# Kernel optimization log

Hardware: AMD Instinct MI355X
Metric: run time of the kernel (lower is better)

Reference implementation:

```python
import jax, jax.numpy as jnp
import numpy as np

B, C, H, W = 1, 12, 256, 256
T = 8          # time_steps
F = 64         # recurrent/conv filters
SIGMA = 1.0


def _to_c(x):
    return jax.lax.complex(x[..., 0], x[..., 1])


def _to_r(x):
    return jnp.stack([jnp.real(x), jnp.imag(x)], axis=-1)


def _fft2c(x):  # orthogonal centered 2D FFT over last two dims (complex input)
    x = jnp.fft.ifftshift(x, axes=(-2, -1))
    x = jnp.fft.fft2(x, axes=(-2, -1), norm='ortho')
    return jnp.fft.fftshift(x, axes=(-2, -1))


def _ifft2c(x):
    x = jnp.fft.ifftshift(x, axes=(-2, -1))
    x = jnp.fft.ifft2(x, axes=(-2, -1), norm='ortho')
    return jnp.fft.fftshift(x, axes=(-2, -1))


def _conv(x, w, b=None, dilation=1):
    k = w.shape[-1]
    pad = dilation * (k - 1) // 2  # 'same' padding as ConvNonlinear
    y = jax.lax.conv_general_dilated(x, w, (1, 1), [(pad, pad), (pad, pad)],
                                     rhs_dilation=(dilation, dilation),
                                     dimension_numbers=('NCHW', 'OIHW', 'NCHW'))
    if b is not None:
        y = y + b[None, :, None, None]
    return y


def _gru(x, h, ih_w, ih_b, hh_w, hh_b):  # ConvGRUCell
    i_r, i_z, i_n = jnp.split(_conv(x, ih_w, ih_b), 3, axis=1)
    h_r, h_z, h_n = jnp.split(_conv(h, hh_w, hh_b), 3, axis=1)
    r = jax.nn.sigmoid(i_r + h_r)
    z = jax.nn.sigmoid(i_z + h_z)
    n = jnp.tanh(i_n + r * h_n)
    return (1.0 - z) * n + z * h


def setup_inputs():
    key = jax.random.key(0)
    ks = jax.random.split(key, 16)
    rn = lambda k, s, sc=1.0: jax.random.normal(k, s, jnp.float32) * sc
    return {
        'pred': rn(ks[0], (B, C, H, W, 2)),
        'masked_kspace': rn(ks[1], (B, C, H, W, 2)),
        'sense': rn(ks[2], (B, C, H, W, 2), 0.1),
        'mask': jax.random.randint(ks[3], (B, 1, H, W, 1), 0, 2).astype(bool),
        'conv1_w': rn(ks[4], (F, 4, 5, 5), 0.05),
        'conv1_b': jnp.zeros((F,), jnp.float32),
        'gru1_ih_w': rn(ks[5], (3 * F, F, 1, 1), 0.05),
        'gru1_ih_b': jnp.zeros((3 * F,), jnp.float32),
        'gru1_hh_w': rn(ks[6], (3 * F, F, 1, 1), 0.05),
        'gru1_hh_b': jnp.zeros((3 * F,), jnp.float32),
        'conv2_w': rn(ks[7], (F, F, 3, 3), 0.05),
        'conv2_b': jnp.zeros((F,), jnp.float32),
        'gru2_ih_w': rn(ks[8], (3 * F, F, 1, 1), 0.05),
        'gru2_ih_b': jnp.zeros((3 * F,), jnp.float32),
        'gru2_hh_w': rn(ks[9], (3 * F, F, 1, 1), 0.05),
        'gru2_hh_b': jnp.zeros((3 * F,), jnp.float32),
        'final_w': rn(ks[10], (2, F, 3, 3), 0.05),
        'dc_weight': jnp.ones((1,), jnp.float32),
    }


def reference(pred, masked_kspace, sense, mask, conv1_w, conv1_b, gru1_ih_w, gru1_ih_b,
              gru1_hh_w, gru1_hh_b, conv2_w, conv2_b, gru2_ih_w, gru2_ih_b, gru2_hh_w,
              gru2_hh_b, final_w, dc_weight):
    ksp_c = _to_c(masked_kspace)   # [B,C,H,W] complex
    sense_c = _to_c(sense)
    mask_f = mask[..., 0].astype(jnp.float32)  # [B,1,H,W]
    # eta init (eta=None path): coil-combined ifft of pred
    eta0 = jnp.sum(_ifft2c(_to_c(pred)) * jnp.conj(sense_c), axis=1)  # [B,H,W]
    h1_0 = jnp.zeros((B, F, H, W), jnp.float32)
    h2_0 = jnp.zeros((B, F, H, W), jnp.float32)
    inv_s2 = 1.0 / (SIGMA * SIGMA)

    def step(carry, _):
        eta, h1, h2 = carry
        # log_likelihood_gradient: SENSE-expand, fft, masked residual, ifft, coil-combine
        resid = _ifft2c(mask_f * (_fft2c(eta[:, None] * sense_c) - ksp_c))  # [B,C,H,W]
        grad = jnp.sum(resid * jnp.conj(sense_c), axis=1)                   # [B,H,W]
        g = jnp.stack([eta.real, eta.imag, grad.real, grad.imag], axis=1) * inv_s2  # [B,4,H,W]
        h1 = _gru(jax.nn.relu(_conv(g, conv1_w, conv1_b, 1)), h1,
                  gru1_ih_w, gru1_ih_b, gru1_hh_w, gru1_hh_b)
        h2 = _gru(jax.nn.relu(_conv(h1, conv2_w, conv2_b, 2)), h2,
                  gru2_ih_w, gru2_ih_b, gru2_hh_w, gru2_hh_b)
        d = _conv(h2, final_w, None, 1)  # [B,2,H,W], no bias, no nonlinearity
        eta = eta + jax.lax.complex(d[:, 0], d[:, 1])
        return (eta, h1, h2), eta

    _, etas = jax.lax.scan(step, (eta0, h1_0, h2_0), None, length=T)  # [T,B,H,W]
    # data-consistency output per time step
    soft_dc = jnp.where(mask, pred - masked_kspace, 0.0) * dc_weight[0]  # [B,C,H,W,2]
    dc_c = _to_c(soft_dc)
    out = ksp_c[None] - dc_c[None] - _fft2c(etas[:, :, None] * sense_c[None])  # [T,B,C,H,W]
    return _to_r(out)  # [T,B,C,H,W,2]
```

## Files before the change

### kernel.cpp

```cpp
#include <hip/hip_runtime.h>

#define HW 65536
#define NC 12
#define NF 64
#define NT 8
#define P2 260

typedef float2 c32;
typedef __attribute__((ext_vector_type(8))) short bf16x8;
typedef __attribute__((ext_vector_type(4))) float f32x4;

__device__ __forceinline__ float ssign(int p) {
    return ((p ^ (p >> 8)) & 1) ? -1.0f : 1.0f;
}

__device__ __forceinline__ short f2bf(float f) {
    union { float f; unsigned u; } v; v.f = f;
    unsigned r = (v.u + 0x7FFFu + ((v.u >> 16) & 1u)) >> 16;
    return (short)r;
}

__device__ __forceinline__ float bf2f(unsigned short u) {
    union { unsigned u; float f; } v; v.u = (unsigned)u << 16;
    return v.f;
}

__device__ __forceinline__ void wave_sync() {
    asm volatile("s_waitcnt lgkmcnt(0)" ::: "memory");
}

__device__ __forceinline__ void fft256_wave(c32* X, const c32* tw, int j, float conjf) {
    #pragma unroll
    for (int s = 1; s <= 8; s += 2) {
        const int H = 1 << (s - 1);
        int p = j & (H - 1);
        int r = j >> (s - 1);
        int i0 = r * 4 * H + p;
        c32 e0 = X[i0], e1 = X[i0 + H], e2 = X[i0 + 2 * H], e3 = X[i0 + 3 * H];
        c32 w = tw[p << (8 - s)];
        float wy = conjf * w.y;
        c32 t = make_float2(w.x * e1.x - wy * e1.y, w.x * e1.y + wy * e1.x);
        c32 a0 = make_float2(e0.x + t.x, e0.y + t.y);
        c32 a1 = make_float2(e0.x - t.x, e0.y - t.y);
        t = make_float2(w.x * e3.x - wy * e3.y, w.x * e3.y + wy * e3.x);
        c32 a2 = make_float2(e2.x + t.x, e2.y + t.y);
        c32 a3 = make_float2(e2.x - t.x, e2.y - t.y);
        c32 w0 = tw[p << (7 - s)];
        c32 w1 = tw[(p + H) << (7 - s)];
        float w0y = conjf * w0.y, w1y = conjf * w1.y;
        t = make_float2(w0.x * a2.x - w0y * a2.y, w0.x * a2.y + w0y * a2.x);
        X[i0]         = make_float2(a0.x + t.x, a0.y + t.y);
        X[i0 + 2 * H] = make_float2(a0.x - t.x, a0.y - t.y);
        t = make_float2(w1.x * a3.x - w1y * a3.y, w1.x * a3.y + w1y * a3.x);
        X[i0 + H]     = make_float2(a1.x + t.x, a1.y + t.y);
        X[i0 + 3 * H] = make_float2(a1.x - t.x, a1.y - t.y);
        wave_sync();
    }
}

__device__ __forceinline__ void fft256_2w(c32* X, const c32* tw, int lane, float conjf) {
    #pragma unroll
    for (int s = 1; s <= 8; ++s) {
        const int half = 1 << (s - 1);
        int grp = lane >> (s - 1);
        int pos = lane & (half - 1);
        int i0 = (grp << s) + pos;
        int i1 = i0 + half;
        c32 w = tw[pos << (8 - s)];
        float wy = conjf * w.y;
        c32 a = X[i0], cc = X[i1];
        c32 t = make_float2(w.x * cc.x - wy * cc.y, w.x * cc.y + wy * cc.x);
        X[i0] = make_float2(a.x + t.x, a.y + t.y);
        X[i1] = make_float2(a.x - t.x, a.y - t.y);
        __syncthreads();
    }
}

__device__ __forceinline__ void build_tw(c32* tw, int tid) {
    if (tid < 128) {
        float a = -3.14159265358979323846f * (float)tid * (1.0f / 128.0f);
        float sv, cv;
        sincosf(a, &sv, &cv);
        tw[tid] = make_float2(cv, sv);
    }
}

__global__ __launch_bounds__(256) void fft_rows_pre(c32* __restrict__ buf,
        const c32* __restrict__ pred) {
    __shared__ c32 lds[2][256];
    __shared__ c32 tw[128];
    int tid = threadIdx.x;
    build_tw(tw, tid);
    int li = tid >> 7, lane = tid & 127;
    int r = blockIdx.x * 2 + li;
    int coil = r >> 8, y = r & 255;
    c32* rp = buf + (size_t)r * 256;
    c32* X = lds[li];
    #pragma unroll
    for (int e = 0; e < 2; ++e) {
        int n = (e << 7) + lane;
        float s = ((n + y) & 1) ? -1.0f : 1.0f;
        c32 pv = pred[(size_t)coil * HW + y * 256 + n];
        X[__brev((unsigned)n) >> 24] = make_float2(s * pv.x, s * pv.y);
    }
    __syncthreads();
    fft256_2w(X, tw, lane, -1.0f);
    #pragma unroll
    for (int e = 0; e < 2; ++e) {
        int n = (e << 7) + lane;
        rp[n] = X[n];
    }
}

__global__ __launch_bounds__(256) void fft_rows_exp(c32* __restrict__ buf,
        const c32* __restrict__ eta, const c32* __restrict__ sense) {
    __shared__ c32 lds[2][256];
    __shared__ c32 tw[128];
    int tid = threadIdx.x;
    build_tw(tw, tid);
    int li = tid >> 7, lane = tid & 127;
    int r = blockIdx.x * 2 + li;
    int coil = r >> 8, y = r & 255;
    c32* rp = buf + (size_t)r * 256;
    c32* X = lds[li];
    #pragma unroll
    for (int e = 0; e < 2; ++e) {
        int n = (e << 7) + lane;
        float s = ((n + y) & 1) ? -1.0f : 1.0f;
        c32 ev = eta[y * 256 + n];
        c32 sn = sense[(size_t)coil * HW + y * 256 + n];
        X[__brev((unsigned)n) >> 24] =
            make_float2(s * (ev.x * sn.x - ev.y * sn.y),
                        s * (ev.x * sn.y + ev.y * sn.x));
    }
    __syncthreads();
    fft256_2w(X, tw, lane, 1.0f);
    #pragma unroll
    for (int e = 0; e < 2; ++e) {
        int n = (e << 7) + lane;
        rp[n] = X[n];
    }
}

__global__ __launch_bounds__(768) void final_exp(const short* __restrict__ hTp,
        const short* __restrict__ wA, c32* __restrict__ eta,
        const c32* __restrict__ sense, c32* __restrict__ buf) {
    __shared__ c32 X[12][256];
    __shared__ c32 tw[128];
    __shared__ float erx[256], ery[256];
    int tid = threadIdx.x;
    build_tw(tw, tid);
    int wv = tid >> 6, l = tid & 63;
    int lr = l & 15, lg = l >> 4;
    int y = blockIdx.x;

    for (int tile = wv; tile < 16; tile += 12) {
        int x = tile * 16 + lr;
        f32x4 C = (f32x4){0.f, 0.f, 0.f, 0.f};
        #pragma unroll
        for (int tap = 0; tap < 9; ++tap) {
            int dy = tap / 3 - 1, dx = tap % 3 - 1;
            const short* pA = wA + (size_t)(tap * 16 + lr) * 64 + lg * 8;
            bf16x8 A0 = *(const bf16x8*)(pA);
            bf16x8 A1 = *(const bf16x8*)(pA + 32);
            const short* pB = hTp +
                ((size_t)((y + dy + 2) * P2 + (x + dx + 2)) << 6) + lg * 8;
            bf16x8 B0 = *(const bf16x8*)(pB);
            bf16x8 B1 = *(const bf16x8*)(pB + 32);
            C = __builtin_amdgcn_mfma_f32_16x16x32_bf16(A0, B0, C, 0, 0, 0);
            C = __builtin_amdgcn_mfma_f32_16x16x32_bf16(A1, B1, C, 0, 0, 0);
        }
        if (lg == 0) {
            int px = y * 256 + x;
            c32 e = eta[px];
            float ex = e.x + C[0], ey = e.y + C[1];
            eta[px] = make_float2(ex, ey);
            erx[x] = ex; ery[x] = ey;
        }
    }
    __syncthreads();

    {
        c32* Xc = &X[wv][0];
        const c32* sn = sense + (size_t)wv * HW + y * 256;
        #pragma unroll
        for (int e = 0; e < 4; ++e) {
            int n = (e << 6) + l;
            float s = ((n + y) & 1) ? -1.0f : 1.0f;
            float ex = erx[n], ey = ery[n];
            c32 sv = sn[n];
            Xc[__brev((unsigned)n) >> 24] =
                make_float2(s * (ex * sv.x - ey * sv.y),
                            s * (ex * sv.y + ey * sv.x));
        }
        wave_sync();
        fft256_wave(Xc, tw, l, 1.0f);
        c32* rp = buf + (size_t)wv * HW + y * 256;
        #pragma unroll
        for (int e = 0; e < 4; ++e) {
            int n = (e << 6) + l;
            rp[n] = Xc[n];
        }
    }
}

__global__ __launch_bounds__(768) void fft_rows_grad(const c32* __restrict__ Fk,
        const c32* __restrict__ sense, const c32* __restrict__ eta,
        short* __restrict__ gTp) {
    __shared__ c32 lds[12][256];
    __shared__ c32 tw[128];
    int tid = threadIdx.x;
    build_tw(tw, tid);
    int wid = tid >> 6, j = tid & 63;
    int y = blockIdx.x;
    {
        const c32* rp = Fk + (size_t)wid * HW + y * 256;
        #pragma unroll
        for (int e = 0; e < 4; ++e) {
            int n = (e << 6) + j;
            lds[wid][__brev((unsigned)n) >> 24] = rp[n];
        }
    }
    __syncthreads();
    fft256_wave(&lds[wid][0], tw, j, -1.0f);
    __syncthreads();
    if (tid < 256) {
        int x = tid;
        int p = y * 256 + x;
        float ax = 0.f, ay = 0.f;
        #pragma unroll
        for (int c = 0; c < NC; ++c) {
            c32 t = lds[c][x];
            c32 s = sense[(size_t)c * HW + p];
            ax += t.x * s.x + t.y * s.y;
            ay += t.y * s.x - t.x * s.y;
        }
        float sc = (((x + y) & 1) ? -1.0f : 1.0f) * (1.0f / 256.0f);
        c32 e = eta[p];
        ushort4 o;
        o.x = (unsigned short)f2bf(e.x);
        o.y = (unsigned short)f2bf(e.y);
        o.z = (unsigned short)f2bf(ax * sc);
        o.w = (unsigned short)f2bf(ay * sc);
        ((ushort4*)gTp)[(y + 2) * P2 + x + 2] = o;
    }
}

__global__ __launch_bounds__(1024) void fft_cols(c32* __restrict__ buf, float conjf) {
    __shared__ c32 lds[8][257];
    __shared__ c32 tw[128];
    int tid = threadIdx.x;
    build_tw(tw, tid);
    c32* ip = buf + (size_t)blockIdx.y * HW;
    int x0 = blockIdx.x * 8;
    int xl = tid & 7, yb = tid >> 3;
    #pragma unroll
    for (int e = 0; e < 2; ++e) {
        int y = yb + (e << 7);
        lds[xl][__brev((unsigned)y) >> 24] = ip[y * 256 + x0 + xl];
    }
    __syncthreads();
    int col = tid >> 7, lane = tid & 127;
    fft256_2w(&lds[col][0], tw, lane, conjf);
    #pragma unroll
    for (int e = 0; e < 2; ++e) {
        int y = yb + (e << 7);
        ip[y * 256 + x0 + xl] = lds[xl][y];
    }
}

__global__ __launch_bounds__(1024) void fft_cols_fused(c32* __restrict__ buf,
        const c32* __restrict__ base, const c32* __restrict__ ksp,
        const int* __restrict__ mask, c32* __restrict__ outp, int write_out) {
    __shared__ c32 lds[8][257];
    __shared__ c32 tw[128];
    int tid = threadIdx.x;
    build_tw(tw, tid);
    int coil = blockIdx.y;
    c32* ip = buf + (size_t)coil * HW;
    int x0 = blockIdx.x * 8;
    int xl = tid & 7, yb = tid >> 3;
    #pragma unroll
    for (int e = 0; e < 2; ++e) {
        int y = yb + (e << 7);
        lds[xl][__brev((unsigned)y) >> 24] = ip[y * 256 + x0 + xl];
    }
    __syncthreads();
    int col = tid >> 7, lane = tid & 127;
    fft256_2w(&lds[col][0], tw, lane, 1.0f);

    int x = x0 + xl;
    c32 G[2];
    #pragma unroll
    for (int e = 0; e < 2; ++e) {
        int y = yb + (e << 7);
        G[e] = lds[xl][y];
    }
    __syncthreads();
    #pragma unroll
    for (int e = 0; e < 2; ++e) {
        int y = yb + (e << 7);
        int p = y * 256 + x;
        size_t i = (size_t)coil * HW + p;
        float s = ((p ^ (p >> 8)) & 1) ? -1.0f : 1.0f;
        if (write_out) {
            c32 bv = base[i];
            float sc = s * (1.0f / 256.0f);
            outp[i] = make_float2(bv.x - sc * G[e].x, bv.y - sc * G[e].y);
        }
        c32 rv = make_float2(0.f, 0.f);
        if (mask[p]) {
            c32 k = ksp[i];
            rv = make_float2(G[e].x * (1.0f / 256.0f) - s * k.x,
                             G[e].y * (1.0f / 256.0f) - s * k.y);
        }
        lds[xl][__brev((unsigned)y) >> 24] = rv;
    }
    __syncthreads();
    fft256_2w(&lds[col][0], tw, lane, -1.0f);
    #pragma unroll
    for (int e = 0; e < 2; ++e) {
        int y = yb + (e << 7);
        ip[y * 256 + x0 + xl] = lds[xl][y];
    }
}

__global__ __launch_bounds__(256) void k_combine_eta0(const c32* __restrict__ tmp,
        const c32* __restrict__ sense, c32* __restrict__ eta) {
    int p = blockIdx.x * 256 + threadIdx.x;
    float ax = 0.f, ay = 0.f;
    for (int c = 0; c < NC; ++c) {
        c32 t = tmp[c * HW + p], s = sense[c * HW + p];
        ax += t.x * s.x + t.y * s.y;
        ay += t.y * s.x - t.x * s.y;
    }
    float sc = ssign(p) * (1.0f / 256.0f);
    eta[p] = make_float2(ax * sc, ay * sc);
}

__global__ __launch_bounds__(256) void k_base(const c32* __restrict__ ksp,
        const c32* __restrict__ pred, const int* __restrict__ mask,
        const float* __restrict__ dcw, c32* __restrict__ base) {
    int i = blockIdx.x * 256 + threadIdx.x;
    int p = i & (HW - 1);
    c32 k = ksp[i];
    c32 o = k;
    if (mask[p]) {
        float w = dcw[0];
        c32 pr = pred[i];
        o.x -= (pr.x - k.x) * w;
        o.y -= (pr.y - k.y) * w;
    }
    base[i] = o;
}

__global__ __launch_bounds__(256) void k_zero_border(short* __restrict__ gTp,
        short* __restrict__ h1a, short* __restrict__ h1b,
        short* __restrict__ h2a, short* __restrict__ h2b) {
    int i = blockIdx.x * 256 + threadIdx.x;
    if (i >= 2064) return;
    int y, x;
    if (i < 1040) {
        int r = i / 260;
        y = (r < 2) ? r : 256 + r;
        x = i % 260;
    } else {
        int j = i - 1040;
        y = 2 + (j >> 2);
        int cix = j & 3;
        x = (cix < 2) ? cix : 256 + cix;
    }
    size_t px = (size_t)y * P2 + x;
    ((ushort4*)gTp)[px] = make_ushort4(0, 0, 0, 0);
    uint4 z = make_uint4(0, 0, 0, 0);
    uint4* p1 = (uint4*)(h1a + (px << 6));
    uint4* p2 = (uint4*)(h1b + (px << 6));
    uint4* p3 = (uint4*)(h2a + (px << 6));
    uint4* p4 = (uint4*)(h2b + (px << 6));
    #pragma unroll
    for (int e = 0; e < 8; ++e) { p1[e] = z; p2[e] = z; p3[e] = z; p4[e] = z; }
}

__global__ __launch_bounds__(256) void k_prep_c1(const float* __restrict__ w,
        short* __restrict__ wA) {
    int i = blockIdx.x * 256 + threadIdx.x;
    int co = i >> 7, k = i & 127;
    int tap = k >> 2, ci = k & 3;
    float v = (tap < 25) ? w[co * 100 + ci * 25 + tap] : 0.f;
    wA[i] = f2bf(v);
}

__global__ __launch_bounds__(256) void k_prep_c2(const float* __restrict__ w,
        short* __restrict__ wA) {
    int i = blockIdx.x * 256 + threadIdx.x;
    int tap = i >> 12, co = (i >> 6) & 63, ci = i & 63;
    wA[i] = f2bf(w[co * 576 + ci * 9 + tap]);
}

__global__ __launch_bounds__(256) void k_prep_cf(const float* __restrict__ w,
        short* __restrict__ wA) {
    int i = blockIdx.x * 256 + threadIdx.x;
    int tap = i >> 10, r = (i >> 6) & 15, ci = i & 63;
    float v = (r < 2) ? w[r * 576 + ci * 9 + tap] : 0.f;
    wA[i] = f2bf(v);
}

__global__ __launch_bounds__(128) void k_prep_gru(const float* __restrict__ ihw,
        const float* __restrict__ ihb, const float* __restrict__ hhw,
        const float* __restrict__ hhb, short* __restrict__ w2, float* __restrict__ bias) {
    int k = threadIdx.x;
    int r = blockIdx.x;
    int g = r >> 6, co = r & 63;
    float v = 0.f;
    if (g == 0)      v = (k < 64) ? ihw[co * 64 + k]         : hhw[co * 64 + k - 64];
    else if (g == 1) v = (k < 64) ? ihw[(64 + co) * 64 + k]  : hhw[(64 + co) * 64 + k - 64];
    else if (g == 2) v = (k < 64) ? ihw[(128 + co) * 64 + k] : 0.f;
    else             v = (k < 64) ? 0.f : hhw[(128 + co) * 64 + k - 64];
    w2[r * 128 + k] = f2bf(v);
    if (k == 0) {
        float b = (g == 0) ? ihb[co] + hhb[co]
                : (g == 1) ? ihb[64 + co] + hhb[64 + co]
                : (g == 2) ? ihb[128 + co] : hhb[128 + co];
        bias[r] = b;
    }
}

template <int NTN, bool FIRST>
__device__ __forceinline__ void gru_tail(const short (*xch)[68],
        const short* __restrict__ hprev, const short* __restrict__ w2,
        const float* __restrict__ bias, short* __restrict__ hnext,
        int wv, int lr, int lg, int px0) {
    bf16x8 A0[4], A1[4], A2[2], A3[2];
    {
        const short* w0 = w2 + (0   + wv * 16 + lr) * 128 + lg * 8;
        const short* w1 = w2 + (64  + wv * 16 + lr) * 128 + lg * 8;
        const short* w2p = w2 + (128 + wv * 16 + lr) * 128 + lg * 8;
        const short* w3 = w2 + (192 + wv * 16 + lr) * 128 + lg * 8;
        #pragma unroll
        for (int kt = 0; kt < 4; ++kt) {
            A0[kt] = *(const bf16x8*)(w0 + kt * 32);
            A1[kt] = *(const bf16x8*)(w1 + kt * 32);
        }
        A2[0] = *(const bf16x8*)(w2p);          A2[1] = *(const bf16x8*)(w2p + 32);
        A3[0] = *(const bf16x8*)(w3 + 64);      A3[1] = *(const bf16x8*)(w3 + 96);
    }

    f32x4 C0[NTN], C1[NTN], C2[NTN], C3[NTN];
    #pragma unroll
    for (int nt = 0; nt < NTN; ++nt) {
        C0[nt] = (f32x4){0.f, 0.f, 0.f, 0.f};
        C1[nt] = (f32x4){0.f, 0.f, 0.f, 0.f};
        C2[nt] = (f32x4){0.f, 0.f, 0.f, 0.f};
        C3[nt] = (f32x4){0.f, 0.f, 0.f, 0.f};
    }

    #pragma unroll
    for (int nt = 0; nt < NTN; ++nt) {
        int pxl = nt * 16 + lr;
        int px = px0 + pxl;
        int yy = px >> 8, xx = px & 255;
        size_t pb = ((size_t)((yy + 2) * P2 + (xx + 2)) << 6);
        bf16x8 B0 = *(const bf16x8*)&xch[pxl][lg * 8];
        bf16x8 B1 = *(const bf16x8*)&xch[pxl][32 + lg * 8];
        C0[nt] = __builtin_amdgcn_mfma_f32_16x16x32_bf16(A0[0], B0, C0[nt], 0, 0, 0);
        C0[nt] = __builtin_amdgcn_mfma_f32_16x16x32_bf16(A0[1], B1, C0[nt], 0, 0, 0);
        C1[nt] = __builtin_amdgcn_mfma_f32_16x16x32_bf16(A1[0], B0, C1[nt], 0, 0, 0);
        C1[nt] = __builtin_amdgcn_mfma_f32_16x16x32_bf16(A1[1], B1, C1[nt], 0, 0, 0);
        C2[nt] = __builtin_amdgcn_mfma_f32_16x16x32_bf16(A2[0], B0, C2[nt], 0, 0, 0);
        C2[nt] = __builtin_amdgcn_mfma_f32_16x16x32_bf16(A2[1], B1, C2[nt], 0, 0, 0);
        if (!FIRST) {
            bf16x8 B2 = *(const bf16x8*)(hprev + pb + lg * 8);
            bf16x8 B3 = *(const bf16x8*)(hprev + pb + 32 + lg * 8);
            C0[nt] = __builtin_amdgcn_mfma_f32_16x16x32_bf16(A0[2], B2, C0[nt], 0, 0, 0);
            C0[nt] = __builtin_amdgcn_mfma_f32_16x16x32_bf16(A0[3], B3, C0[nt], 0, 0, 0);
            C1[nt] = __builtin_amdgcn_mfma_f32_16x16x32_bf16(A1[2], B2, C1[nt], 0, 0, 0);
            C1[nt] = __builtin_amdgcn_mfma_f32_16x16x32_bf16(A1[3], B3, C1[nt], 0, 0, 0);
            C3[nt] = __builtin_amdgcn_mfma_f32_16x16x32_bf16(A3[0], B2, C3[nt], 0, 0, 0);
            C3[nt] = __builtin_amdgcn_mfma_f32_16x16x32_bf16(A3[1], B3, C3[nt], 0, 0, 0);
        }
    }

    int co = wv * 16 + lg * 4;
    float br[4], bz[4], bin_[4], bhn[4];
    #pragma unroll
    for (int i = 0; i < 4; ++i) {
        br[i]   = bias[co + i];
        bz[i]   = bias[64 + co + i];
        bin_[i] = bias[128 + co + i];
        bhn[i]  = bias[192 + co + i];
    }
    #pragma unroll
    for (int nt = 0; nt < NTN; ++nt) {
        int px = px0 + nt * 16 + lr;
        int yy = px >> 8, xx = px & 255;
        size_t pb = ((size_t)((yy + 2) * P2 + (xx + 2)) << 6);
        ushort4 hov = make_ushort4(0, 0, 0, 0);
        if (!FIRST) hov = *(const ushort4*)(hprev + pb + co);
        float ho[4] = {bf2f(hov.x), bf2f(hov.y), bf2f(hov.z), bf2f(hov.w)};
        ushort4 st;
        unsigned short* sp = &st.x;
        #pragma unroll
        for (int i = 0; i < 4; ++i) {
            float r = 1.0f / (1.0f + expf(-(C0[nt][i] + br[i])));
            float z = 1.0f / (1.0f + expf(-(C1[nt][i] + bz[i])));
            float nn = tanhf(C2[nt][i] + bin_[i] + r * (C3[nt][i] + bhn[i]));
            float hv = FIRST ? (1.0f - z) * nn : (1.0f - z) * nn + z * ho[i];
            sp[i] = (unsigned short)f2bf(hv);
        }
        *(ushort4*)(hnext + pb + co) = st;
    }
}

template <bool FIRST>
__global__ __launch_bounds__(256, 2) void conv1_gru1(const short* __restrict__ gTp,
        const short* __restrict__ wA, const float* __restrict__ cbias,
        const short* __restrict__ w2, const float* __restrict__ gbias,
        const short* __restrict__ hprev, short* __restrict__ hnext) {
    __shared__ short xch[32][68];
    int wv = threadIdx.x >> 6, l = threadIdx.x & 63;
    int lr = l & 15, lg = l >> 4;
    int y = blockIdx.x >> 3;
    int x0 = (blockIdx.x & 7) << 5;

    bf16x8 A[4];
    const short* pA = wA + (size_t)(wv * 16 + lr) * 128 + lg * 8;
    #pragma unroll
    for (int kt = 0; kt < 4; ++kt) A[kt] = *(const bf16x8*)(pA + kt * 32);

    bf16x8 B[2][4];
    #pragma unroll
    for (int nt = 0; nt < 2; ++nt) {
        int x = x0 + nt * 16 + lr;
        #pragma unroll
        for (int kt = 0; kt < 4; ++kt) {
            int t0 = kt * 8 + lg * 2;
            #pragma unroll
            for (int half = 0; half < 2; ++half) {
                int tap = t0 + half;
                int tt = (tap < 25) ? tap : 0;
                int dy = tt / 5 - 2, dx = tt % 5 - 2;
                ushort4 v = *(const ushort4*)(gTp +
                    ((size_t)((y + dy + 2) * P2 + (x + dx + 2)) << 2));
                B[nt][kt][half * 4 + 0] = (short)v.x;
                B[nt][kt][half * 4 + 1] = (short)v.y;
                B[nt][kt][half * 4 + 2] = (short)v.z;
                B[nt][kt][half * 4 + 3] = (short)v.w;
            }
        }
    }
    int co = wv * 16 + lg * 4;
    #pragma unroll
    for (int nt = 0; nt < 2; ++nt) {
        f32x4 C = (f32x4){0.f, 0.f, 0.f, 0.f};
        #pragma unroll
        for (int kt = 0; kt < 4; ++kt)
            C = __builtin_amdgcn_mfma_f32_16x16x32_bf16(A[kt], B[nt][kt], C, 0, 0, 0);
        ushort4 st;
        st.x = (unsigned short)f2bf(fmaxf(C[0] + cbias[co + 0], 0.f));
        st.y = (unsigned short)f2bf(fmaxf(C[1] + cbias[co + 1], 0.f));
        st.z = (unsigned short)f2bf(fmaxf(C[2] + cbias[co + 2], 0.f));
        st.w = (unsigned short)f2bf(fmaxf(C[3] + cbias[co + 3], 0.f));
        *(ushort4*)&xch[nt * 16 + lr][co] = st;
    }
    __syncthreads();

    gru_tail<2, FIRST>(xch, hprev, w2, gbias, hnext, wv, lr, lg, y * 256 + x0);
}

template <bool FIRST>
__global__ __launch_bounds__(256, 2) void conv2_gru2(const short* __restrict__ h1Tp,
        const short* __restrict__ wA, const float* __restrict__ cbias,
        const short* __restrict__ w2, const float* __restrict__ gbias,
        const short* __restrict__ hprev, short* __restrict__ hnext) {
    __shared__ uint4 Ld[3][68][9];
    __shared__ short xch[64][68];
    int tid = threadIdx.x;
    int wv = tid >> 6, l = tid & 63;
    int lr = l & 15, lg = l >> 4;
    int y = blockIdx.x >> 2;
    int x0 = (blockIdx.x & 3) << 6;

    for (int n = tid; n < 3 * 68 * 8; n += 256) {
        int r = n / (68 * 8);
        int rem = n - r * (68 * 8);
        int px = rem >> 3, e = rem & 7;
        const uint4* src = (const uint4*)(h1Tp +
            (((size_t)(y + 2 * r) * P2 + (x0 + px)) << 6)) + e;
        Ld[r][px][e] = *src;
    }
    __syncthreads();

    f32x4 C[4];
    #pragma unroll
    for (int nt = 0; nt < 4; ++nt) C[nt] = (f32x4){0.f, 0.f, 0.f, 0.f};

    #pragma unroll
    for (int tap = 0; tap < 9; ++tap) {
        int r = tap / 3;
        int dx = (tap % 3 - 1) * 2;
        const short* pA = wA + (size_t)(tap * 64 + wv * 16 + lr) * 64 + lg * 8;
        bf16x8 A0 = *(const bf16x8*)(pA);
        bf16x8 A1 = *(const bf16x8*)(pA + 32);
        #pragma unroll
        for (int nt = 0; nt < 4; ++nt) {
            int xl = nt * 16 + lr + dx + 2;
            bf16x8 B0 = *(const bf16x8*)&Ld[r][xl][lg];
            bf16x8 B1 = *(const bf16x8*)&Ld[r][xl][4 + lg];
            C[nt] = __builtin_amdgcn_mfma_f32_16x16x32_bf16(A0, B0, C[nt], 0, 0, 0);
            C[nt] = __builtin_amdgcn_mfma_f32_16x16x32_bf16(A1, B1, C[nt], 0, 0, 0);
        }
    }
    int co = wv * 16 + lg * 4;
    #pragma unroll
    for (int nt = 0; nt < 4; ++nt) {
        ushort4 st;
        st.x = (unsigned short)f2bf(fmaxf(C[nt][0] + cbias[co + 0], 0.f));
        st.y = (unsigned short)f2bf(fmaxf(C[nt][1] + cbias[co + 1], 0.f));
        st.z = (unsigned short)f2bf(fmaxf(C[nt][2] + cbias[co + 2], 0.f));
        st.w = (unsigned short)f2bf(fmaxf(C[nt][3] + cbias[co + 3], 0.f));
        *(ushort4*)&xch[nt * 16 + lr][co] = st;
    }
    __syncthreads();

    gru_tail<4, FIRST>(xch, hprev, w2, gbias, hnext, wv, lr, lg, y * 256 + x0);
}

extern "C" void kernel_launch(void* const* d_in, const int* in_sizes, int n_in,
                              void* d_out, int out_size, void* d_ws, size_t ws_size,
                              hipStream_t stream) {
    const c32* pred   = (const c32*)d_in[0];
    const c32* ksp    = (const c32*)d_in[1];
    const c32* sense  = (const c32*)d_in[2];
    const int* mask   = (const int*)d_in[3];
    const float* c1w  = (const float*)d_in[4];
    const float* c1b  = (const float*)d_in[5];
    const float* g1iw = (const float*)d_in[6];
    const float* g1ib = (const float*)d_in[7];
    const float* g1hw = (const float*)d_in[8];
    const float* g1hb = (const float*)d_in[9];
    const float* c2w  = (const float*)d_in[10];
    const float* c2b  = (const float*)d_in[11];
    const float* g2iw = (const float*)d_in[12];
    const float* g2ib = (const float*)d_in[13];
    const float* g2hw = (const float*)d_in[14];
    const float* g2hb = (const float*)d_in[15];
    const float* fw   = (const float*)d_in[16];
    const float* dcw  = (const float*)d_in[17];

    const size_t PP = (size_t)P2 * P2;
    float* w0 = (float*)d_ws;
    c32* base = (c32*)w0;
    c32* Fk   = base + NC * HW;
    c32* tmp  = Fk + NC * HW;
    c32* eta  = tmp + NC * HW;
    short* gTp = (short*)(eta + HW);
    short* h1Ta = gTp + PP * 4;
    short* h1Tb = h1Ta + PP * 64;
    short* h2Ta = h1Tb + PP * 64;
    short* h2Tb = h2Ta + PP * 64;
    short* w2a  = h2Tb + PP * 64;
    short* w2b  = w2a + 256 * 128;
    float* biasA = (float*)(w2b + 256 * 128);
    float* biasB = biasA + 256;
    short* wAc2 = (short*)(biasB + 256);
    short* wAc1 = wAc2 + 9 * 64 * 64;
    short* wAcf = wAc1 + 64 * 128;

    dim3 B(256);
    const int gCHW = NC * HW / 256;
    const int gHW  = HW / 256;
    const int gROW = NC * 256 / 2;
    dim3 gCOL(32, NC);
    dim3 B1024(1024);
    dim3 B768(768);
    const int gC1 = HW / 32;
    const int gC2 = HW / 64;

    k_zero_border<<<9, B, 0, stream>>>(gTp, h1Ta, h1Tb, h2Ta, h2Tb);
    k_prep_gru<<<256, 128, 0, stream>>>(g1iw, g1ib, g1hw, g1hb, w2a, biasA);
    k_prep_gru<<<256, 128, 0, stream>>>(g2iw, g2ib, g2hw, g2hb, w2b, biasB);
    k_prep_c2<<<144, 256, 0, stream>>>(c2w, wAc2);
    k_prep_c1<<<32, 256, 0, stream>>>(c1w, wAc1);
    k_prep_cf<<<36, 256, 0, stream>>>(fw, wAcf);

    fft_rows_pre<<<gROW, B, 0, stream>>>(tmp, pred);
    fft_cols<<<gCOL, B1024, 0, stream>>>(tmp, -1.0f);
    k_combine_eta0<<<gHW, B, 0, stream>>>(tmp, sense, eta);

    k_base<<<gCHW, B, 0, stream>>>(ksp, pred, mask, dcw, base);

    fft_rows_exp<<<gROW, B, 0, stream>>>(Fk, eta, sense);
    fft_cols_fused<<<gCOL, B1024, 0, stream>>>(Fk, base, ksp, mask, (c32*)d_out, 0);

    short* h1c = h1Ta; short* h1n = h1Tb;
    short* h2c = h2Ta; short* h2n = h2Tb;
    c32* outp = (c32*)d_out;

    for (int t = 0; t < NT; ++t) {
        fft_rows_grad<<<gHW, B768, 0, stream>>>(Fk, sense, eta, gTp);

        if (t == 0) {
            conv1_gru1<true><<<gC1, B, 0, stream>>>(gTp, wAc1, c1b, w2a, biasA, h1c, h1n);
        } else {
            conv1_gru1<false><<<gC1, B, 0, stream>>>(gTp, wAc1, c1b, w2a, biasA, h1c, h1n);
        }
        { short* s = h1c; h1c = h1n; h1n = s; }
        if (t == 0) {
            conv2_gru2<true><<<gC2, B, 0, stream>>>(h1c, wAc2, c2b, w2b, biasB, h2c, h2n);
        } else {
            conv2_gru2<false><<<gC2, B, 0, stream>>>(h1c, wAc2, c2b, w2b, biasB, h2c, h2n);
        }
        { short* s = h2c; h2c = h2n; h2n = s; }

        final_exp<<<gHW, B768, 0, stream>>>(h2c, wAcf, eta, sense, Fk);

        fft_cols_fused<<<gCOL, B1024, 0, stream>>>(Fk, base, ksp, mask,
                                                   outp + (size_t)t * NC * HW, 1);
    }
}
```

Measured before the change: 853.0 us.

## Store k-space intermediate and sense maps as packed bf16 complex

Stores the per-coil k-space intermediate buffer (Fk) and a precomputed copy of the sense maps as packed bf16 pairs, one 32-bit word per complex value, in place of float2. All row/column FFT kernels in the loop now read and write half the bytes. The aim is to cut global memory traffic in these bandwidth-bound FFT passes. The cost is lower precision in the FFT intermediates and coil combination, which can affect accuracy of the outputs written at each step.

```diff
diff --git a/kernel.cpp b/kernel.cpp
--- a/kernel.cpp
+++ b/kernel.cpp
@@ -23,6 +23,16 @@
 __device__ __forceinline__ float bf2f(unsigned short u) {
     union { unsigned u; float f; } v; v.u = (unsigned)u << 16;
     return v.f;
+}
+
+__device__ __forceinline__ unsigned pack_bf(float x, float y) {
+    return (unsigned)(unsigned short)f2bf(x) |
+           ((unsigned)(unsigned short)f2bf(y) << 16);
+}
+
+__device__ __forceinline__ c32 unpack_bf(unsigned u) {
+    return make_float2(bf2f((unsigned short)(u & 0xffff)),
+                       bf2f((unsigned short)(u >> 16)));
 }
 
 __device__ __forceinline__ void wave_sync() {
@@ -112,7 +122,7 @@
     }
 }
 
-__global__ __launch_bounds__(256) void fft_rows_exp(c32* __restrict__ buf,
+__global__ __launch_bounds__(256) void fft_rows_exp(unsigned* __restrict__ buf,
         const c32* __restrict__ eta, const c32* __restrict__ sense) {
     __shared__ c32 lds[2][256];
     __shared__ c32 tw[128];
@@ -121,7 +131,7 @@
     int li = tid >> 7, lane = tid & 127;
     int r = blockIdx.x * 2 + li;
     int coil = r >> 8, y = r & 255;
-    c32* rp = buf + (size_t)r * 256;
+    unsigned* rp = buf + (size_t)r * 256;
     c32* X = lds[li];
     #pragma unroll
     for (int e = 0; e < 2; ++e) {
@@ -138,13 +148,13 @@
     #pragma unroll
     for (int e = 0; e < 2; ++e) {
         int n = (e << 7) + lane;
-        rp[n] = X[n];
+        rp[n] = pack_bf(X[n].x, X[n].y);
     }
 }
 
 __global__ __launch_bounds__(768) void final_exp(const short* __restrict__ hTp,
         const short* __restrict__ wA, c32* __restrict__ eta,
-        const c32* __restrict__ sense, c32* __restrict__ buf) {
+        const unsigned* __restrict__ senseb, unsigned* __restrict__ buf) {
     __shared__ c32 X[12][256];
     __shared__ c32 tw[128];
     __shared__ float erx[256], ery[256];
@@ -182,30 +192,30 @@
 
     {
         c32* Xc = &X[wv][0];
-        const c32* sn = sense + (size_t)wv * HW + y * 256;
+        const unsigned* sn = senseb + (size_t)wv * HW + y * 256;
         #pragma unroll
         for (int e = 0; e < 4; ++e) {
             int n = (e << 6) + l;
             float s = ((n + y) & 1) ? -1.0f : 1.0f;
             float ex = erx[n], ey = ery[n];
-            c32 sv = sn[n];
+            c32 sv = unpack_bf(sn[n]);
             Xc[__brev((unsigned)n) >> 24] =
                 make_float2(s * (ex * sv.x - ey * sv.y),
                             s * (ex * sv.y + ey * sv.x));
         }
         wave_sync();
         fft256_wave(Xc, tw, l, 1.0f);
-        c32* rp = buf + (size_t)wv * HW + y * 256;
+        unsigned* rp = buf + (size_t)wv * HW + y * 256;
         #pragma unroll
         for (int e = 0; e < 4; ++e) {
             int n = (e << 6) + l;
-            rp[n] = Xc[n];
-        }
-    }
-}
-
-__global__ __launch_bounds__(768) void fft_rows_grad(const c32* __restrict__ Fk,
-        const c32* __restrict__ sense, const c32* __restrict__ eta,
+            rp[n] = pack_bf(Xc[n].x, Xc[n].y);
+        }
+    }
+}
+
+__global__ __launch_bounds__(768) void fft_rows_grad(const unsigned* __restrict__ Fk,
+        const unsigned* __restrict__ senseb, const c32* __restrict__ eta,
         short* __restrict__ gTp) {
     __shared__ c32 lds[12][256];
     __shared__ c32 tw[128];
@@ -214,11 +224,11 @@
     int wid = tid >> 6, j = tid & 63;
     int y = blockIdx.x;
     {
-        const c32* rp = Fk + (size_t)wid * HW + y * 256;
+        const unsigned* rp = Fk + (size_t)wid * HW + y * 256;
         #pragma unroll
         for (int e = 0; e < 4; ++e) {
             int n = (e << 6) + j;
-            lds[wid][__brev((unsigned)n) >> 24] = rp[n];
+            lds[wid][__brev((unsigned)n) >> 24] = unpack_bf(rp[n]);
         }
     }
     __syncthreads();
@@ -231,7 +241,7 @@
         #pragma unroll
         for (int c = 0; c < NC; ++c) {
             c32 t = lds[c][x];
-            c32 s = sense[(size_t)c * HW + p];
+            c32 s = unpack_bf(senseb[(size_t)c * HW + p]);
             ax += t.x * s.x + t.y * s.y;
             ay += t.y * s.x - t.x * s.y;
         }
@@ -269,7 +279,7 @@
     }
 }
 
-__global__ __launch_bounds__(1024) void fft_cols_fused(c32* __restrict__ buf,
+__global__ __launch_bounds__(1024) void fft_cols_fused(unsigned* __restrict__ buf,
         const c32* __restrict__ base, const c32* __restrict__ ksp,
         const int* __restrict__ mask, c32* __restrict__ outp, int write_out) {
     __shared__ c32 lds[8][257];
@@ -277,13 +287,13 @@
     int tid = threadIdx.x;
     build_tw(tw, tid);
     int coil = blockIdx.y;
-    c32* ip = buf + (size_t)coil * HW;
+    unsigned* ip = buf + (size_t)coil * HW;
     int x0 = blockIdx.x * 8;
     int xl = tid & 7, yb = tid >> 3;
     #pragma unroll
     for (int e = 0; e < 2; ++e) {
         int y = yb + (e << 7);
-        lds[xl][__brev((unsigned)y) >> 24] = ip[y * 256 + x0 + xl];
+        lds[xl][__brev((unsigned)y) >> 24] = unpack_bf(ip[y * 256 + x0 + xl]);
     }
     __syncthreads();
     int col = tid >> 7, lane = tid & 127;
@@ -321,7 +331,7 @@
     #pragma unroll
     for (int e = 0; e < 2; ++e) {
         int y = yb + (e << 7);
-        ip[y * 256 + x0 + xl] = lds[xl][y];
+        ip[y * 256 + x0 + xl] = pack_bf(lds[xl][y].x, lds[xl][y].y);
     }
 }
 
@@ -352,6 +362,13 @@
         o.y -= (pr.y - k.y) * w;
     }
     base[i] = o;
+}
+
+__global__ __launch_bounds__(256) void k_prep_sense(const c32* __restrict__ sense,
+        unsigned* __restrict__ senseb) {
+    int i = blockIdx.x * 256 + threadIdx.x;
+    c32 s = sense[i];
+    senseb[i] = pack_bf(s.x, s.y);
 }
 
 __global__ __launch_bounds__(256) void k_zero_border(short* __restrict__ gTp,
@@ -650,10 +667,11 @@
     const size_t PP = (size_t)P2 * P2;
     float* w0 = (float*)d_ws;
     c32* base = (c32*)w0;
-    c32* Fk   = base + NC * HW;
-    c32* tmp  = Fk + NC * HW;
+    c32* tmp  = base + NC * HW;
     c32* eta  = tmp + NC * HW;
-    short* gTp = (short*)(eta + HW);
+    unsigned* Fkb = (unsigned*)(eta + HW);
+    unsigned* senseb = Fkb + NC * HW;
+    short* gTp = (short*)(senseb + NC * HW);
     short* h1Ta = gTp + PP * 4;
     short* h1Tb = h1Ta + PP * 64;
     short* h2Ta = h1Tb + PP * 64;
@@ -682,6 +700,7 @@
     k_prep_c2<<<144, 256, 0, stream>>>(c2w, wAc2);
     k_prep_c1<<<32, 256, 0, stream>>>(c1w, wAc1);
     k_prep_cf<<<36, 256, 0, stream>>>(fw, wAcf);
+    k_prep_sense<<<gCHW, B, 0, stream>>>(sense, senseb);
 
     fft_rows_pre<<<gROW, B, 0, stream>>>(tmp, pred);
     fft_cols<<<gCOL, B1024, 0, stream>>>(tmp, -1.0f);
@@ -689,15 +708,15 @@
 
     k_base<<<gCHW, B, 0, stream>>>(ksp, pred, mask, dcw, base);
 
-    fft_rows_exp<<<gROW, B, 0, stream>>>(Fk, eta, sense);
-    fft_cols_fused<<<gCOL, B1024, 0, stream>>>(Fk, base, ksp, mask, (c32*)d_out, 0);
+    fft_rows_exp<<<gROW, B, 0, stream>>>(Fkb, eta, sense);
+    fft_cols_fused<<<gCOL, B1024, 0, stream>>>(Fkb, base, ksp, mask, (c32*)d_out, 0);
 
     short* h1c = h1Ta; short* h1n = h1Tb;
     short* h2c = h2Ta; short* h2n = h2Tb;
     c32* outp = (c32*)d_out;
 
     for (int t = 0; t < NT; ++t) {
-        fft_rows_grad<<<gHW, B768, 0, stream>>>(Fk, sense, eta, gTp);
+        fft_rows_grad<<<gHW, B768, 0, stream>>>(Fkb, senseb, eta, gTp);
 
         if (t == 0) {
             conv1_gru1<true><<<gC1, B, 0, stream>>>(gTp, wAc1, c1b, w2a, biasA, h1c, h1n);
@@ -712,9 +731,9 @@
         }
         { short* s = h2c; h2c = h2n; h2n = s; }
 
-        final_exp<<<gHW, B768, 0, stream>>>(h2c, wAcf, eta, sense, Fk);
-
-        fft_cols_fused<<<gCOL, B1024, 0, stream>>>(Fk, base, ksp, mask,
+        final_exp<<<gHW, B768, 0, stream>>>(h2c, wAcf, eta, senseb, Fkb);
+
+        fft_cols_fused<<<gCOL, B1024, 0, stream>>>(Fkb, base, ksp, mask,
                                                    outp + (size_t)t * NC * HW, 1);
     }
 }
```

Result: no change. 847.0 us (-0.7%).
